# Performance work log

Hardware: AMD Instinct MI355X
Metric: run time of the kernel (lower is better)

## Reference

```python
import jax, jax.numpy as jnp
import numpy as np
from jax import lax

B, N, C = 8, 16384, 4
NUM_GROUPS = 128
GROUP_SIZE = 32
GROUP_RADIUS = 0.1
UPSCALE_K = 128
OVERLAP_FACTOR = 0.7


def setup_inputs() -> dict:
    key = jax.random.key(0)
    k1, k2 = jax.random.split(key)
    # xyz in [0,1]^3, energy in [0,1] at channel 3
    points = jax.random.uniform(k1, (B, N, C), dtype=jnp.float32)
    lengths = jax.random.randint(k2, (B,), N // 2, N + 1).astype(jnp.int32)
    return {"points": points, "lengths": lengths}


def _fps(xyz, lengths, K):
    """Farthest point sampling. xyz: (B,N,3) -> centers (B,K,3), idx (B,K)."""
    B_, N_, _ = xyz.shape
    valid = jnp.arange(N_)[None, :] < lengths[:, None]          # (B,N)
    mind0 = jnp.where(valid, jnp.inf, -jnp.inf)                 # running min dist
    start = jnp.zeros((B_,), jnp.int32)                         # fixed start point
    batch = jnp.arange(B_)

    def step(carry, _):
        mind, cur = carry
        c = xyz[batch, cur]                                     # (B,3)
        d = jnp.sum((xyz - c[:, None, :]) ** 2, axis=-1)        # (B,N)
        mind = jnp.minimum(mind, jnp.where(valid, d, -jnp.inf))
        nxt = jnp.argmax(mind, axis=1).astype(jnp.int32)
        return (mind, nxt), cur

    _, idxs = lax.scan(step, (mind0, start), None, length=K)
    idxs = idxs.T                                               # (B,K)
    centers = xyz[batch[:, None], idxs]                         # (B,K,3)
    return centers, idxs


def _cnms(centers, radius, overlap_factor):
    """Greedy cluster-NMS over FPS-ordered centers. Returns keep mask (B,G)."""
    B_, G, _ = centers.shape
    d2 = jnp.sum((centers[:, :, None, :] - centers[:, None, :, :]) ** 2, axis=-1)
    thr = (2.0 * radius * (1.0 - overlap_factor)) ** 2          # spheres overlap > factor

    def step(keep, j):
        conflict = jnp.any(keep & (d2[:, j, :] < thr), axis=-1)
        keep = keep.at[:, j].set(~conflict)
        return keep, None

    keep, _ = lax.scan(step, jnp.zeros((B_, G), bool), jnp.arange(G))
    return keep


def _ball_query(centers, xyz, lengths, retain, K, radius):
    """First-K points within radius of each center (pytorch3d semantics); -1 pad."""
    N_ = xyz.shape[1]
    d2 = jnp.sum((centers[:, :, None, :] - xyz[:, None, :, :]) ** 2, axis=-1)  # (B,G,N)
    in_len = (jnp.arange(N_)[None, :] < lengths[:, None])[:, None, :]
    valid = (d2 <= radius * radius) & in_len & retain[:, :, None]
    # pick the K smallest point indices among valid ones -> "first K found"
    key_ = jnp.where(valid, jnp.arange(N_, dtype=jnp.int32)[None, None, :], N_)
    negv, _ = lax.top_k(-key_, K)                               # (B,G,K)
    idx = -negv
    return jnp.where(idx == N_, -1, idx)


def reference(points, lengths):
    xyz = points[..., :3]
    centers, _ = _fps(xyz, lengths, NUM_GROUPS)                 # (B,G,3)
    retain = _cnms(centers, GROUP_RADIUS, OVERLAP_FACTOR)       # (B,G)
    idx = _ball_query(centers, xyz, lengths, retain, UPSCALE_K, GROUP_RADIUS)

    # select_topk_by_energy (energies_idx = 3)
    batch = jnp.arange(points.shape[0])[:, None, None]
    invalid = idx == -1
    energies = jnp.where(invalid, -jnp.inf, points[batch, jnp.clip(idx, 0), 3])
    topv, topi = lax.top_k(energies, GROUP_SIZE)                # (B,G,K_new)
    tidx = jnp.take_along_axis(idx, topi, axis=2)
    tidx = jnp.where(jnp.isneginf(topv), -1, tidx)

    # fill_empty_indices: replace -1 with the group's first index
    fidx = jnp.where(tidx == -1, tidx[:, :, :1], tidx)

    # masked_gather: -1 -> gather 0 then zero out
    groups = points[batch, jnp.clip(fidx, 0)]                   # (B,G,K,C)
    groups = jnp.where((fidx == -1)[..., None], 0.0, groups)

    group_lengths = jnp.sum(jnp.all(tidx != -1, axis=2), axis=1)  # (B,)
    embedding_mask = jnp.arange(NUM_GROUPS)[None, :] < group_lengths[:, None]

    # center xyz channels, then scale ALL channels by radius (as in source)
    groups = groups.at[..., :3].add(-centers[:, :, None, :])
    groups = groups / GROUP_RADIUS
    return groups, centers, embedding_mask
```

## Files before the change

### kernel.cpp

```cpp
#include <hip/hip_runtime.h>
#include <math.h>

#define B_ 8
#define N_ 16384
#define G_ 128
#define GS_ 32
#define UK_ 128
#define FPS_T 512
#define FPS_W 8
#define FPS_BLK 4
#define SLICE (N_ / FPS_BLK)
#define PPT (SLICE / FPS_T)
#define BQ_T 512
#define BQ_W 8

#pragma clang fp contract(off)

typedef float v2f __attribute__((ext_vector_type(2)));

#define DPP64_MAXSTEP(vv, ctrl, rmask)                                          \
  {                                                                             \
    unsigned _lo = (unsigned)__builtin_amdgcn_update_dpp(                       \
        0, (int)(unsigned)((vv) & 0xffffffffull), (ctrl), (rmask), 0xf, false); \
    unsigned _hi = (unsigned)__builtin_amdgcn_update_dpp(                       \
        0, (int)(unsigned)((vv) >> 32), (ctrl), (rmask), 0xf, false);           \
    unsigned long long _tv = ((unsigned long long)_hi << 32) | _lo;             \
    if (_tv > (vv)) (vv) = _tv;                                                 \
  }

__device__ __forceinline__ unsigned long long shfl_xor_u64(unsigned long long v, int m) {
    int lo = __shfl_xor((int)(unsigned)(v & 0xffffffffull), m);
    int hi = __shfl_xor((int)(unsigned)(v >> 32), m);
    return ((unsigned long long)(unsigned)hi << 32) | (unsigned)lo;
}

__device__ __forceinline__ unsigned long long umax64(unsigned long long a,
                                                     unsigned long long b) {
    return a > b ? a : b;
}

__device__ __forceinline__ float dist2(float x, float y, float z,
                                       float cx, float cy, float cz) {
    float dx = __fsub_rn(x, cx);
    float dy = __fsub_rn(y, cy);
    float dz = __fsub_rn(z, cz);
    return __fadd_rn(__fadd_rn(__fmul_rn(dx, dx), __fmul_rn(dy, dy)),
                     __fmul_rn(dz, dz));
}

__global__ void init_kernel(unsigned long long* __restrict__ slots,
                            int* __restrict__ gl) {
    int t = threadIdx.x;
#pragma unroll
    for (int i = 0; i < (B_ * G_ * FPS_BLK) / 1024; i++)
        slots[i * 1024 + t] = 0ull;
    if (t < B_) gl[t] = 0;
}

__global__ __launch_bounds__(FPS_T, 2) void fps_cnms_kernel(
    const float4* __restrict__ pts, const int* __restrict__ lengths,
    float* __restrict__ centers_out, int* __restrict__ keep_out,
    unsigned long long* __restrict__ slots) {
    const int b = blockIdx.x & 7;
    const int slice = blockIdx.x >> 3;
    const int t = threadIdx.x;
    const int lane = t & 63;
    const int wv = t >> 6;
    const int len = lengths[b];
    const float4* p = pts + (size_t)b * N_;
    const int base = slice * SLICE;

    __shared__ __align__(16) unsigned long long s_part[2][FPS_W];
    __shared__ float s_cen[G_][3];

    v2f xp[PPT / 2], yp[PPT / 2], zp[PPT / 2];
    v2f mp[PPT / 2];
#pragma unroll
    for (int j = 0; j < PPT / 2; j += 2) {
        int nA0 = base + (2 * j) * FPS_T + t;
        float4 qA0, qB0, qA1, qB1;
        const float4* a0 = p + nA0;
        const float4* b0 = a0 + FPS_T;
        const float4* a1 = a0 + 2 * FPS_T;
        const float4* b1 = a0 + 3 * FPS_T;
        asm volatile(
            "global_load_dwordx4 %0, %4, off\n\t"
            "global_load_dwordx4 %1, %5, off\n\t"
            "global_load_dwordx4 %2, %6, off\n\t"
            "global_load_dwordx4 %3, %7, off\n\t"
            "s_waitcnt vmcnt(0)"
            : "=&v"(qA0), "=&v"(qB0), "=&v"(qA1), "=&v"(qB1)
            : "v"(a0), "v"(b0), "v"(a1), "v"(b1)
            : "memory");
        xp[j]     = (v2f){qA0.x, qB0.x};
        yp[j]     = (v2f){qA0.y, qB0.y};
        zp[j]     = (v2f){qA0.z, qB0.z};
        xp[j + 1] = (v2f){qA1.x, qB1.x};
        yp[j + 1] = (v2f){qA1.y, qB1.y};
        zp[j + 1] = (v2f){qA1.z, qB1.z};
        v2f mm0, mm1;
        mm0.x = (nA0 < len)             ? INFINITY : -INFINITY;
        mm0.y = (nA0 + FPS_T < len)     ? INFINITY : -INFINITY;
        mm1.x = (nA0 + 2 * FPS_T < len) ? INFINITY : -INFINITY;
        mm1.y = (nA0 + 3 * FPS_T < len) ? INFINITY : -INFINITY;
        mp[j] = mm0;
        mp[j + 1] = mm1;
    }

    int n = 0;
    for (int k = 0; k < G_; k++) {
        float4 c = p[n];
        if (slice == 0 && t == 0) {
            centers_out[(b * G_ + k) * 3 + 0] = c.x;
            centers_out[(b * G_ + k) * 3 + 1] = c.y;
            centers_out[(b * G_ + k) * 3 + 2] = c.z;
            s_cen[k][0] = c.x; s_cen[k][1] = c.y; s_cen[k][2] = c.z;
        }
        if (k == G_ - 1) break;

        v2f cXX = {c.x, c.x};
        v2f cYY = {c.y, c.y};
        v2f cZZ = {c.z, c.z};

#pragma unroll
        for (int j = 0; j < PPT / 2; j++) {
            v2f dx = xp[j] - cXX;
            v2f dy = yp[j] - cYY;
            v2f dz = zp[j] - cZZ;
            v2f dd = (dx * dx + dy * dy) + dz * dz;
            mp[j] = __builtin_elementwise_min(mp[j], dd);
        }

        v2f t2a = __builtin_elementwise_max(mp[0], mp[1]);
        v2f t2b = __builtin_elementwise_max(mp[2], mp[3]);
        v2f t1  = __builtin_elementwise_max(t2a, t2b);
        float bv = fmaxf(t1.x, t1.y);

        int bi = 0;
#pragma unroll
        for (int j = PPT / 2 - 1; j >= 0; j--) {
            bool hx = (mp[j].x == bv);
            bool hy = (mp[j].y == bv);
            int cand = 2 * j + (hx ? 0 : 1);
            if (hx || hy) bi = cand;
        }

        unsigned u = __float_as_uint(bv);
        u = (u & 0x80000000u) ? ~u : (u | 0x80000000u);
        int bn = base | (bi << 9) | t;
        unsigned long long v = ((unsigned long long)u << 32) | (unsigned)(~bn);

        DPP64_MAXSTEP(v, 0x111, 0xf);
        DPP64_MAXSTEP(v, 0x112, 0xf);
        DPP64_MAXSTEP(v, 0x114, 0xf);
        DPP64_MAXSTEP(v, 0x118, 0xf);
        DPP64_MAXSTEP(v, 0x142, 0xa);
        DPP64_MAXSTEP(v, 0x143, 0xc);
        if (lane == 63) s_part[k & 1][wv] = v;
        __syncthreads();

        unsigned long long m = s_part[k & 1][lane & 7];
        DPP64_MAXSTEP(m, 0x111, 0xf);
        DPP64_MAXSTEP(m, 0x112, 0xf);
        DPP64_MAXSTEP(m, 0x114, 0xf);
        unsigned klo = (unsigned)__builtin_amdgcn_readlane(
            (int)(unsigned)(m & 0xffffffffull), 7);
        unsigned khi = (unsigned)__builtin_amdgcn_readlane(
            (int)(unsigned)(m >> 32), 7);
        unsigned long long kk = ((unsigned long long)khi << 32) | klo;

        unsigned long long* slot = slots + ((size_t)b * G_ + k) * FPS_BLK;
        if (wv == 0 && lane == 0)
            __hip_atomic_store(&slot[slice], kk, __ATOMIC_RELAXED,
                               __HIP_MEMORY_SCOPE_AGENT);
        unsigned long long pv = kk;
        if (lane < FPS_BLK && lane != slice) {
            do {
                pv = __hip_atomic_load(&slot[lane], __ATOMIC_RELAXED,
                                       __HIP_MEMORY_SCOPE_AGENT);
            } while (pv == 0ull);
        }
        unsigned long long mg = umax64(pv, shfl_xor_u64(pv, 1));
        mg = umax64(mg, shfl_xor_u64(mg, 2));
        unsigned wlo = (unsigned)__builtin_amdgcn_readfirstlane(
            (int)(unsigned)(mg & 0xffffffffull));
        n = (int)(~wlo);
    }

    __syncthreads();

    if (slice == 0 && t < 64) {
        const float THR = (float)((2.0 * 0.1 * (1.0 - 0.7)) * (2.0 * 0.1 * (1.0 - 0.7)));
        float ax = s_cen[t][0],      ay = s_cen[t][1],      az = s_cen[t][2];
        float ex = s_cen[t + 64][0], ey = s_cen[t + 64][1], ez = s_cen[t + 64][2];
        bool k0 = false, k1 = false;
        for (int j = 0; j < G_; j++) {
            float jx = s_cen[j][0], jy = s_cen[j][1], jz = s_cen[j][2];
            bool c0 = k0 && (dist2(ax, ay, az, jx, jy, jz) < THR);
            bool c1 = k1 && (dist2(ex, ey, ez, jx, jy, jz) < THR);
            bool conflict = __any(c0 || c1);
            if (j == t)      k0 = !conflict;
            if (j == t + 64) k1 = !conflict;
        }
        keep_out[b * G_ + t]      = k0 ? 1 : 0;
        keep_out[b * G_ + t + 64] = k1 ? 1 : 0;
    }
}

__global__ __launch_bounds__(BQ_T) void group_kernel(
    const float4* __restrict__ pts, const int* __restrict__ lengths,
    const float* __restrict__ centers, const int* __restrict__ keep,
    float* __restrict__ groups_out, int* __restrict__ gl) {
    const int bid = blockIdx.x;
    const int b = bid >> 7;
    const int t = threadIdx.x;
    const int lane = t & 63;
    const int wv = t >> 6;

    const float cx = centers[bid * 3 + 0];
    const float cy = centers[bid * 3 + 1];
    const float cz = centers[bid * 3 + 2];
    float4* out4 = (float4*)(groups_out + (size_t)bid * GS_ * 4);

    if (!keep[bid]) {
        if (t < GS_) {
            float4 o;
            o.x = __fdiv_rn(__fsub_rn(0.f, cx), 0.1f);
            o.y = __fdiv_rn(__fsub_rn(0.f, cy), 0.1f);
            o.z = __fdiv_rn(__fsub_rn(0.f, cz), 0.1f);
            o.w = 0.f;
            out4[t] = o;
        }
        return;
    }

    __shared__ int   s_widx[BQ_W][UK_];
    __shared__ float s_wen[BQ_W][UK_];
    __shared__ int   s_wcnt[BQ_W];
    __shared__ int   s_list[UK_];
    __shared__ float s_en[UK_];
    __shared__ int   s_ord[GS_];

    const int len = lengths[b];
    const float R2 = (float)(0.1 * 0.1);
    const float4* p = pts + (size_t)b * N_;

    {
        const int base0 = wv * (N_ / BQ_W);
        int cnt = 0;
        for (int it = 0; it < (N_ / BQ_W) / 64; it++) {
            int n = base0 + it * 64 + lane;
            float4 q = p[n];
            float d2 = dist2(q.x, q.y, q.z, cx, cy, cz);
            bool pred = (n < len) && (d2 <= R2);
            unsigned long long m = __ballot(pred);
            int prefix = __popcll(m & ((1ull << lane) - 1ull));
            int slot = cnt + prefix;
            if (pred && slot < UK_) { s_widx[wv][slot] = n; s_wen[wv][slot] = q.w; }
            cnt += __popcll(m);
        }
        if (lane == 0) s_wcnt[wv] = (cnt < UK_) ? cnt : UK_;
    }
    __syncthreads();

    int M = 0;
#pragma unroll
    for (int w = 0; w < BQ_W; w++) M += s_wcnt[w];
    if (M > UK_) M = UK_;

    if (t < UK_ && t < M) {
        int j = t, w = 0;
        while (w < BQ_W - 1 && j >= s_wcnt[w]) { j -= s_wcnt[w]; w++; }
        s_list[t] = s_widx[w][j];
        s_en[t]   = s_wen[w][j];
    }
    __syncthreads();

    if (wv == 0) {
        float v0 = (lane < M) ? s_en[lane] : -INFINITY;
        float v1 = (lane + 64 < M) ? s_en[lane + 64] : -INFINITY;
        for (int k = 0; k < GS_; k++) {
            float bv; int bs;
            if (v0 >= v1) { bv = v0; bs = lane; }
            else          { bv = v1; bs = lane + 64; }
#pragma unroll
            for (int off = 32; off; off >>= 1) {
                float ov = __shfl_xor(bv, off);
                int   os = __shfl_xor(bs, off);
                bool tk = (ov > bv) || (ov == bv && os < bs);
                bv = tk ? ov : bv; bs = tk ? os : bs;
            }
            if (lane == 0) s_ord[k] = (bv == -INFINITY) ? -1 : bs;
            if (bs == lane)           v0 = -INFINITY;
            else if (bs == lane + 64) v1 = -INFINITY;
        }
    }
    __syncthreads();

    if (t < GS_) {
        int o0 = s_ord[0];
        int first = (o0 >= 0) ? s_list[o0] : -1;
        int ok = s_ord[t];
        int ti = (ok >= 0) ? s_list[ok] : -1;
        int f = (ti == -1) ? first : ti;
        float px = 0.f, py = 0.f, pz = 0.f, pw = 0.f;
        if (f >= 0) { float4 q = p[f]; px = q.x; py = q.y; pz = q.z; pw = q.w; }
        float4 o;
        o.x = __fdiv_rn(__fsub_rn(px, cx), 0.1f);
        o.y = __fdiv_rn(__fsub_rn(py, cy), 0.1f);
        o.z = __fdiv_rn(__fsub_rn(pz, cz), 0.1f);
        o.w = __fdiv_rn(pw, 0.1f);
        out4[t] = o;
    }
    if (t == 0 && M >= GS_) atomicAdd(&gl[b], 1);
}

__global__ void mask_kernel(const int* __restrict__ gl, float* __restrict__ mask_out) {
    int t = threadIdx.x;
    int b = t >> 7, g = t & 127;
    mask_out[t] = (g < gl[b]) ? 1.0f : 0.0f;
}

extern "C" void kernel_launch(void* const* d_in, const int* in_sizes, int n_in,
                              void* d_out, int out_size, void* d_ws, size_t ws_size,
                              hipStream_t stream) {
    const float4* pts = (const float4*)d_in[0];
    const int* lengths = (const int*)d_in[1];
    float* out = (float*)d_out;
    float* groups = out;
    float* centers = out + (size_t)B_ * G_ * GS_ * 4;
    float* mask = centers + (size_t)B_ * G_ * 3;
    unsigned long long* slots = (unsigned long long*)d_ws;
    int* keep = (int*)(slots + B_ * G_ * FPS_BLK);
    int* gl = keep + B_ * G_;

    hipLaunchKernelGGL(init_kernel, dim3(1), dim3(1024), 0, stream, slots, gl);
    hipLaunchKernelGGL(fps_cnms_kernel, dim3(B_ * FPS_BLK), dim3(FPS_T), 0, stream,
                       pts, lengths, centers, keep, slots);
    hipLaunchKernelGGL(group_kernel, dim3(B_ * G_), dim3(BQ_T), 0, stream,
                       pts, lengths, centers, keep, groups, gl);
    hipLaunchKernelGGL(mask_kernel, dim3(1), dim3(B_ * G_), 0, stream, gl, mask);
}
```

Before: 292.0 us.

## Exchange winning point coordinates through cross-block slots instead of reloading by index

In the multi-block FPS loop, the winning thread of each block now publishes its candidate's xyz coordinates, each tagged with the 32-bit max-distance key, into per-slice slots. Peer blocks read these coordinates directly rather than only learning the index and then reloading the point from global memory. This removes a dependent global load from the serialized per-iteration critical path. In exchange there are three atomic stores and loads per slice instead of one, and ties are now broken by slice order using the local index.

```diff
diff --git a/kernel.cpp b/kernel.cpp
--- a/kernel.cpp
+++ b/kernel.cpp
@@ -17,6 +17,7 @@
 #pragma clang fp contract(off)
 
 typedef float v2f __attribute__((ext_vector_type(2)));
+typedef unsigned long long u64;
 
 #define DPP64_MAXSTEP(vv, ctrl, rmask)                                          \
   {                                                                             \
@@ -24,20 +25,9 @@
         0, (int)(unsigned)((vv) & 0xffffffffull), (ctrl), (rmask), 0xf, false); \
     unsigned _hi = (unsigned)__builtin_amdgcn_update_dpp(                       \
         0, (int)(unsigned)((vv) >> 32), (ctrl), (rmask), 0xf, false);           \
-    unsigned long long _tv = ((unsigned long long)_hi << 32) | _lo;             \
+    u64 _tv = ((u64)_hi << 32) | _lo;                                           \
     if (_tv > (vv)) (vv) = _tv;                                                 \
   }
-
-__device__ __forceinline__ unsigned long long shfl_xor_u64(unsigned long long v, int m) {
-    int lo = __shfl_xor((int)(unsigned)(v & 0xffffffffull), m);
-    int hi = __shfl_xor((int)(unsigned)(v >> 32), m);
-    return ((unsigned long long)(unsigned)hi << 32) | (unsigned)lo;
-}
-
-__device__ __forceinline__ unsigned long long umax64(unsigned long long a,
-                                                     unsigned long long b) {
-    return a > b ? a : b;
-}
 
 __device__ __forceinline__ float dist2(float x, float y, float z,
                                        float cx, float cy, float cz) {
@@ -48,11 +38,10 @@
                      __fmul_rn(dz, dz));
 }
 
-__global__ void init_kernel(unsigned long long* __restrict__ slots,
-                            int* __restrict__ gl) {
+__global__ void init_kernel(u64* __restrict__ slots, int* __restrict__ gl) {
     int t = threadIdx.x;
 #pragma unroll
-    for (int i = 0; i < (B_ * G_ * FPS_BLK) / 1024; i++)
+    for (int i = 0; i < (B_ * G_ * FPS_BLK * 4) / 1024; i++)
         slots[i * 1024 + t] = 0ull;
     if (t < B_) gl[t] = 0;
 }
@@ -60,7 +49,7 @@
 __global__ __launch_bounds__(FPS_T, 2) void fps_cnms_kernel(
     const float4* __restrict__ pts, const int* __restrict__ lengths,
     float* __restrict__ centers_out, int* __restrict__ keep_out,
-    unsigned long long* __restrict__ slots) {
+    u64* __restrict__ slots) {
     const int b = blockIdx.x & 7;
     const int slice = blockIdx.x >> 3;
     const int t = threadIdx.x;
@@ -70,7 +59,7 @@
     const float4* p = pts + (size_t)b * N_;
     const int base = slice * SLICE;
 
-    __shared__ __align__(16) unsigned long long s_part[2][FPS_W];
+    __shared__ __align__(16) u64 s_part[2][FPS_W];
     __shared__ float s_cen[G_][3];
 
     v2f xp[PPT / 2], yp[PPT / 2], zp[PPT / 2];
@@ -107,20 +96,21 @@
         mp[j + 1] = mm1;
     }
 
-    int n = 0;
+    float4 c0 = p[0];
+    float cx = c0.x, cy = c0.y, cz = c0.z;
+
     for (int k = 0; k < G_; k++) {
-        float4 c = p[n];
         if (slice == 0 && t == 0) {
-            centers_out[(b * G_ + k) * 3 + 0] = c.x;
-            centers_out[(b * G_ + k) * 3 + 1] = c.y;
-            centers_out[(b * G_ + k) * 3 + 2] = c.z;
-            s_cen[k][0] = c.x; s_cen[k][1] = c.y; s_cen[k][2] = c.z;
+            centers_out[(b * G_ + k) * 3 + 0] = cx;
+            centers_out[(b * G_ + k) * 3 + 1] = cy;
+            centers_out[(b * G_ + k) * 3 + 2] = cz;
+            s_cen[k][0] = cx; s_cen[k][1] = cy; s_cen[k][2] = cz;
         }
         if (k == G_ - 1) break;
 
-        v2f cXX = {c.x, c.x};
-        v2f cYY = {c.y, c.y};
-        v2f cZZ = {c.z, c.z};
+        v2f cXX = {cx, cx};
+        v2f cYY = {cy, cy};
+        v2f cZZ = {cz, cz};
 
 #pragma unroll
         for (int j = 0; j < PPT / 2; j++) {
@@ -147,8 +137,8 @@
 
         unsigned u = __float_as_uint(bv);
         u = (u & 0x80000000u) ? ~u : (u | 0x80000000u);
-        int bn = base | (bi << 9) | t;
-        unsigned long long v = ((unsigned long long)u << 32) | (unsigned)(~bn);
+        int bn = (bi << 9) | t;
+        u64 v = ((u64)u << 32) | (unsigned)(~bn);
 
         DPP64_MAXSTEP(v, 0x111, 0xf);
         DPP64_MAXSTEP(v, 0x112, 0xf);
@@ -159,7 +149,7 @@
         if (lane == 63) s_part[k & 1][wv] = v;
         __syncthreads();
 
-        unsigned long long m = s_part[k & 1][lane & 7];
+        u64 m = s_part[k & 1][lane & 7];
         DPP64_MAXSTEP(m, 0x111, 0xf);
         DPP64_MAXSTEP(m, 0x112, 0xf);
         DPP64_MAXSTEP(m, 0x114, 0xf);
@@ -167,24 +157,70 @@
             (int)(unsigned)(m & 0xffffffffull), 7);
         unsigned khi = (unsigned)__builtin_amdgcn_readlane(
             (int)(unsigned)(m >> 32), 7);
-        unsigned long long kk = ((unsigned long long)khi << 32) | klo;
-
-        unsigned long long* slot = slots + ((size_t)b * G_ + k) * FPS_BLK;
-        if (wv == 0 && lane == 0)
-            __hip_atomic_store(&slot[slice], kk, __ATOMIC_RELAXED,
+
+        unsigned kb = ~klo;
+        u64* slot = slots + (((size_t)b * G_ + k) * FPS_BLK + slice) * 4;
+        if (t == (int)(kb & 511)) {
+            int bis = (kb >> 9) & 7;
+            v2f sx = (bis & 4) ? ((bis & 2) ? xp[3] : xp[2])
+                               : ((bis & 2) ? xp[1] : xp[0]);
+            v2f sy = (bis & 4) ? ((bis & 2) ? yp[3] : yp[2])
+                               : ((bis & 2) ? yp[1] : yp[0]);
+            v2f sz = (bis & 4) ? ((bis & 2) ? zp[3] : zp[2])
+                               : ((bis & 2) ? zp[1] : zp[0]);
+            float wx = (bis & 1) ? sx.y : sx.x;
+            float wy = (bis & 1) ? sy.y : sy.x;
+            float wz = (bis & 1) ? sz.y : sz.x;
+            u64 ax = ((u64)__float_as_uint(wx) << 32) | khi;
+            u64 ay = ((u64)__float_as_uint(wy) << 32) | khi;
+            u64 az = ((u64)__float_as_uint(wz) << 32) | khi;
+            __hip_atomic_store(&slot[0], ax, __ATOMIC_RELAXED,
                                __HIP_MEMORY_SCOPE_AGENT);
-        unsigned long long pv = kk;
-        if (lane < FPS_BLK && lane != slice) {
+            __hip_atomic_store(&slot[1], ay, __ATOMIC_RELAXED,
+                               __HIP_MEMORY_SCOPE_AGENT);
+            __hip_atomic_store(&slot[2], az, __ATOMIC_RELAXED,
+                               __HIP_MEMORY_SCOPE_AGENT);
+        }
+
+        unsigned tag = 0; float wx = 0.f, wy = 0.f, wz = 0.f; int slc = 3;
+        if (lane < FPS_BLK) {
+            const u64* s3 = slots + (((size_t)b * G_ + k) * FPS_BLK + lane) * 4;
+            u64 ax, ay, az;
             do {
-                pv = __hip_atomic_load(&slot[lane], __ATOMIC_RELAXED,
+                ax = __hip_atomic_load(&s3[0], __ATOMIC_RELAXED,
                                        __HIP_MEMORY_SCOPE_AGENT);
-            } while (pv == 0ull);
-        }
-        unsigned long long mg = umax64(pv, shfl_xor_u64(pv, 1));
-        mg = umax64(mg, shfl_xor_u64(mg, 2));
-        unsigned wlo = (unsigned)__builtin_amdgcn_readfirstlane(
-            (int)(unsigned)(mg & 0xffffffffull));
-        n = (int)(~wlo);
+                ay = __hip_atomic_load(&s3[1], __ATOMIC_RELAXED,
+                                       __HIP_MEMORY_SCOPE_AGENT);
+                az = __hip_atomic_load(&s3[2], __ATOMIC_RELAXED,
+                                       __HIP_MEMORY_SCOPE_AGENT);
+            } while (((unsigned)ax == 0u) | ((unsigned)ay == 0u) |
+                     ((unsigned)az == 0u));
+            tag = (unsigned)ax;
+            wx = __uint_as_float((unsigned)(ax >> 32));
+            wy = __uint_as_float((unsigned)(ay >> 32));
+            wz = __uint_as_float((unsigned)(az >> 32));
+            slc = lane;
+        }
+#pragma unroll
+        for (int mm = 1; mm <= 2; mm <<= 1) {
+            unsigned otag = (unsigned)__shfl_xor((int)tag, mm);
+            int oslc = __shfl_xor(slc, mm);
+            float ox = __shfl_xor(wx, mm);
+            float oy = __shfl_xor(wy, mm);
+            float oz = __shfl_xor(wz, mm);
+            bool take = (otag > tag) || (otag == tag && oslc < slc);
+            tag = take ? otag : tag;
+            slc = take ? oslc : slc;
+            wx = take ? ox : wx;
+            wy = take ? oy : wy;
+            wz = take ? oz : wz;
+        }
+        cx = __uint_as_float((unsigned)__builtin_amdgcn_readfirstlane(
+            (int)__float_as_uint(wx)));
+        cy = __uint_as_float((unsigned)__builtin_amdgcn_readfirstlane(
+            (int)__float_as_uint(wy)));
+        cz = __uint_as_float((unsigned)__builtin_amdgcn_readfirstlane(
+            (int)__float_as_uint(wz)));
     }
 
     __syncthreads();
@@ -330,8 +366,8 @@
     float* groups = out;
     float* centers = out + (size_t)B_ * G_ * GS_ * 4;
     float* mask = centers + (size_t)B_ * G_ * 3;
-    unsigned long long* slots = (unsigned long long*)d_ws;
-    int* keep = (int*)(slots + B_ * G_ * FPS_BLK);
+    u64* slots = (u64*)d_ws;
+    int* keep = (int*)(slots + B_ * G_ * FPS_BLK * 4);
     int* gl = keep + B_ * G_;
 
     hipLaunchKernelGGL(init_kernel, dim3(1), dim3(1024), 0, stream, slots, gl);
```

Measured after the change: 344.0 us. 1.18x slower.
